# Kernel optimization log

Measured on AMD Instinct MI355X. Metric: run time of the kernel, lower is better.

## Reference

```python
import jax, jax.numpy as jnp
import numpy as np

PAD = 0  # module-level global in the original repo (MT convention)


def setup_inputs() -> dict:
    key = jax.random.key(0)
    k1, k2, k3 = jax.random.split(key, 3)
    N, V, D = 2048, 32000, 512
    # realistic log-probabilities over the vocab
    pred_ll = jax.nn.log_softmax(jax.random.normal(k1, (N, V), jnp.float32), axis=-1)
    target = jax.random.randint(k2, (N,), 0, V)
    # frozen pretrained word-vector table (nn.Embedding.from_pretrained)
    emb = jax.random.normal(k3, (V, D), jnp.float32)
    return {"pred_ll": pred_ll, "target": target, "emb": emb}


def reference(pred_ll, target, emb):
    # pred_ll: [N, V] log-probs; target: [N] int ids; emb: [V, D] frozen table
    mask = (target != PAD).astype(pred_ll.dtype)  # [N] non-pad mask

    # nll_loss = -pred_ll.gather(-1, target) summed over non-pad tokens
    nll = -jnp.take_along_axis(pred_ll, target[:, None], axis=-1)[:, 0]  # [N]
    nll_loss = jnp.sum(nll * mask)

    # pairwise L2 distance gold-embedding vs full table, via the GEMM identity
    # ||g - e||^2 = ||g||^2 + ||e||^2 - 2 g.e  (avoids the [N, V, D] tensor)
    g = emb[target]                                    # [N, D]
    g2 = jnp.sum(g * g, axis=-1, keepdims=True)        # [N, 1]
    e2 = jnp.sum(emb * emb, axis=-1)[None, :]          # [1, V]
    d2 = jnp.maximum(g2 + e2 - 2.0 * (g @ emb.T), 0.0)  # [N, V]
    dist = jnp.sqrt(jnp.maximum(d2, 1e-12))             # [N, V], L2 distances

    dist_max = jnp.max(dist, axis=1, keepdims=True)    # [N, 1]
    w = jax.nn.softmax(dist_max - jnp.abs(dist), axis=1)  # [N, V]

    # loss = sum_v softmax_weight * (-log p), summed over non-pad tokens
    loss = jnp.sum(w * (-pred_ll), axis=1)             # [N]
    return (jnp.sum(loss * mask), nll_loss)
```

## Files before the change

kernel.cpp:

```cpp
#include <hip/hip_runtime.h>
#include <float.h>

#define NTOK   2048
#define VOCAB  32000
#define DIM    512
#define NCHUNK 32
#define NTILES 2000
#define ROWSB  64
#define NRB    (NTOK / ROWSB)
#define TILE_BYTES 8192

typedef __attribute__((ext_vector_type(4))) float f32x4;
typedef unsigned int u32;
typedef long long i64;

__device__ __forceinline__ i64 pack_fp8x8(f32x4 x0, f32x4 x1) {
    int lo = __builtin_amdgcn_cvt_pk_fp8_f32(x0.x, x0.y, 0, false);
    lo = __builtin_amdgcn_cvt_pk_fp8_f32(x0.z, x0.w, lo, true);
    int hi = __builtin_amdgcn_cvt_pk_fp8_f32(x1.x, x1.y, 0, false);
    hi = __builtin_amdgcn_cvt_pk_fp8_f32(x1.z, x1.w, hi, true);
    return (i64)(((unsigned long long)(u32)hi << 32) | (u32)lo);
}

__device__ __forceinline__ void async_copy16(void* lds, const void* g) {
    __builtin_amdgcn_global_load_lds(
        (const __attribute__((address_space(1))) u32*)(const u32*)g,
        (__attribute__((address_space(3))) u32*)(u32*)lds, 16, 0, 0);
}

__global__ void init_out(float* out) {
    if (threadIdx.x < 2) out[threadIdx.x] = 0.f;
}

__global__ __launch_bounds__(256) void precast_kernel(
    const float* __restrict__ emb, char* __restrict__ Bbf, float* __restrict__ e2) {
    const int tile = blockIdx.x;
    const int t = threadIdx.x, w = t >> 6, l = t & 63;
    const int v0 = tile * 16;
    char* tbase = Bbf + (size_t)tile * TILE_BYTES;
    #pragma unroll
    for (int it = 0; it < 4; ++it) {
        const int v = it * 4 + w;
        const float* src = emb + (size_t)(v0 + v) * DIM + l * 8;
        f32x4 x0 = *(const f32x4*)src;
        f32x4 x1 = *(const f32x4*)(src + 4);
        float sq = x0.x*x0.x + x0.y*x0.y + x0.z*x0.z + x0.w*x0.w
                 + x1.x*x1.x + x1.y*x1.y + x1.z*x1.z + x1.w*x1.w;
        #pragma unroll
        for (int m = 1; m < 64; m <<= 1) sq += __shfl_xor(sq, m);
        if (l == 0) e2[v0 + v] = sq;
        *(i64*)(tbase + (l >> 2) * 512 + ((l & 3) * 16 + v) * 8) = pack_fp8x8(x0, x1);
    }
}

__global__ __launch_bounds__(256) void e2_kernel(const float* __restrict__ emb,
                                                 float* __restrict__ e2) {
    int gid = blockIdx.x * 256 + threadIdx.x;
    int wid = gid >> 6, l = gid & 63;
    if (wid >= VOCAB) return;
    const float* row = emb + (size_t)wid * DIM + l * 8;
    f32x4 a = *(const f32x4*)row;
    f32x4 b = *(const f32x4*)(row + 4);
    float s = a.x*a.x + a.y*a.y + a.z*a.z + a.w*a.w
            + b.x*b.x + b.y*b.y + b.z*b.z + b.w*b.w;
    #pragma unroll
    for (int m = 1; m < 64; m <<= 1) s += __shfl_xor(s, m);
    if (l == 0) e2[wid] = s;
}

template<bool PRECAST>
__global__ __launch_bounds__(256, 4) void fused_kernel(
    const float* __restrict__ pred_ll, const int* __restrict__ target,
    const float* __restrict__ emb, const char* __restrict__ Bbf,
    const float* __restrict__ e2g,
    float* __restrict__ partials ) {

    const int rb = blockIdx.x;
    const int ch = blockIdx.y;
    const int t  = threadIdx.x;
    const int w  = t >> 6;
    const int l  = t & 63;
    const int l15 = l & 15;
    const int lg  = l >> 4;

    __shared__ char ldsB[2][TILE_BYTES];

    const int t0 = (ch * NTILES) >> 5;
    const int t1 = ((ch + 1) * NTILES) >> 5;
    const int rowbase = rb * ROWSB + w * 16;

    i64 afrag[16];
    {
        const int grow = target[rowbase + l15];
        if constexpr (PRECAST) {
            const char* ab = Bbf + (size_t)(grow >> 4) * TILE_BYTES
                           + ((l & 48) + (grow & 15)) * 8;
            #pragma unroll
            for (int ks = 0; ks < 16; ++ks)
                afrag[ks] = *(const i64*)(ab + ks * 512);
        } else {
            const float* gsrc = emb + (size_t)grow * DIM;
            #pragma unroll
            for (int ks = 0; ks < 16; ++ks) {
                const int k0 = ks * 32 + ((l >> 4) << 3);
                afrag[ks] = pack_fp8x8(*(const f32x4*)(gsrc + k0),
                                       *(const f32x4*)(gsrc + k0 + 4));
            }
        }
    }
    float g2[4];
    #pragma unroll
    for (int r = 0; r < 4; ++r) g2[r] = e2g[target[rowbase + lg * 4 + r]];

    float s_[4] = {0.f, 0.f, 0.f, 0.f};
    float ac_[4] = {0.f, 0.f, 0.f, 0.f};

    auto stage = [&](int buf, int tg) {
        if constexpr (PRECAST) {
            const char* src = Bbf + (size_t)tg * TILE_BYTES;
            async_copy16(ldsB[buf] + t * 16, src + t * 16);
            async_copy16(ldsB[buf] + 4096 + t * 16, src + 4096 + t * 16);
        } else {
            const int v0 = tg * 16;
            #pragma unroll
            for (int it = 0; it < 4; ++it) {
                const int c = it * 256 + t;
                const int ks = c >> 6, il = c & 63;
                const int v = il & 15, k0 = ks * 32 + ((il >> 4) << 3);
                const float* src = emb + (size_t)(v0 + v) * DIM + k0;
                *(i64*)(ldsB[buf] + ks * 512 + il * 8) =
                    pack_fp8x8(*(const f32x4*)src, *(const f32x4*)(src + 4));
            }
        }
    };

    stage(0, t0);

    int cur = 0;
    #pragma unroll 1
    for (int tg = t0; tg < t1; ++tg) {
        if (tg + 1 < t1) {
            stage(cur ^ 1, tg + 1);
            if constexpr (PRECAST)
                asm volatile("s_waitcnt vmcnt(2)" ::: "memory");
            else
                asm volatile("s_waitcnt vmcnt(0) lgkmcnt(0)" ::: "memory");
        } else {
            asm volatile("s_waitcnt vmcnt(0) lgkmcnt(0)" ::: "memory");
        }
        __builtin_amdgcn_s_barrier();

        const int v0 = tg * 16;
        const float e2v = e2g[v0 + l15];
        float q[4];
        {
            const size_t p0 = (size_t)rowbase * VOCAB + v0 + l15;
            #pragma unroll
            for (int r = 0; r < 4; ++r)
                q[r] = pred_ll[p0 + (size_t)(lg * 4 + r) * VOCAB];
        }

        f32x4 acc = {0.f, 0.f, 0.f, 0.f};
        const char* lb = ldsB[cur];
        #pragma unroll
        for (int ks = 0; ks < 16; ++ks) {
            const i64 b = *(const i64*)(lb + ks * 512 + l * 8);
            acc = __builtin_amdgcn_mfma_f32_16x16x32_fp8_fp8(afrag[ks], b, acc, 0, 0, 0);
        }

        #pragma unroll
        for (int r = 0; r < 4; ++r) {
            float d2 = fmaxf(fmaf(-2.f, acc[r], g2[r] + e2v), 1e-12f);
            const float e = __expf(-sqrtf(d2));
            s_[r] += e;
            ac_[r] = fmaf(e, -q[r], ac_[r]);
        }

        asm volatile("" ::: "memory");
        __builtin_amdgcn_s_barrier();
        cur ^= 1;
    }

    #pragma unroll
    for (int r = 0; r < 4; ++r) {
        float sv = s_[r], av = ac_[r];
        #pragma unroll
        for (int m = 1; m < 16; m <<= 1) {
            sv += __shfl_xor(sv, m);
            av += __shfl_xor(av, m);
        }
        if (l15 == 0) {
            const int rg = rowbase + lg * 4 + r;
            float* pp = partials + ((size_t)rg * NCHUNK + ch) * 2;
            pp[0] = sv; pp[1] = av;
        }
    }
}

__global__ __launch_bounds__(256) void reduce_kernel(
    const float* __restrict__ pred_ll, const int* __restrict__ target,
    const float* __restrict__ partials, float* __restrict__ out) {
    const int row = blockIdx.x * 256 + threadIdx.x;
    float loss = 0.f, nll = 0.f;
    if (row < NTOK) {
        const int tg = target[row];
        const float mask = (tg != 0) ? 1.f : 0.f;
        const float* pp = partials + (size_t)row * NCHUNK * 2;
        float S = 0.f, A = 0.f;
        #pragma unroll 8
        for (int c = 0; c < NCHUNK; ++c) { S += pp[c * 2]; A += pp[c * 2 + 1]; }
        loss = mask * (A / S);
        nll  = mask * (-pred_ll[(size_t)row * VOCAB + tg]);
    }
    #pragma unroll
    for (int o = 32; o > 0; o >>= 1) {
        loss += __shfl_xor(loss, o);
        nll  += __shfl_xor(nll, o);
    }
    if ((threadIdx.x & 63) == 0) {
        atomicAdd(&out[0], loss);
        atomicAdd(&out[1], nll);
    }
}

extern "C" void kernel_launch(void* const* d_in, const int* in_sizes, int n_in,
                              void* d_out, int out_size, void* d_ws, size_t ws_size,
                              hipStream_t stream) {
    const float* pred_ll = (const float*)d_in[0];
    const int*   target  = (const int*)d_in[1];
    const float* emb     = (const float*)d_in[2];
    float* out = (float*)d_out;

    float* e2       = (float*)d_ws;
    float* partials = e2 + VOCAB;
    const size_t base = (size_t)VOCAB * 4 + (size_t)NTOK * NCHUNK * 2 * 4;
    char* Bbf       = (char*)d_ws + base;
    const size_t need = base + (size_t)NTILES * TILE_BYTES;
    const bool precast = (ws_size >= need);

    hipLaunchKernelGGL(init_out, dim3(1), dim3(64), 0, stream, out);
    if (precast) {
        hipLaunchKernelGGL(precast_kernel, dim3(NTILES), dim3(256), 0, stream, emb, Bbf, e2);
        hipLaunchKernelGGL((fused_kernel<true>), dim3(NRB, NCHUNK), dim3(256), 0, stream,
                           pred_ll, target, emb, Bbf, e2, partials);
    } else {
        hipLaunchKernelGGL(e2_kernel, dim3(VOCAB * 64 / 256), dim3(256), 0, stream, emb, e2);
        hipLaunchKernelGGL((fused_kernel<false>), dim3(NRB, NCHUNK), dim3(256), 0, stream,
                           pred_ll, target, emb, Bbf, e2, partials);
    }
    hipLaunchKernelGGL(reduce_kernel, dim3(NTOK / 256), dim3(256), 0, stream,
                       pred_ll, target, partials, out);
}
```

Before: 151.1 us.

## Enlarge fused GEMM tile to 32x32 per wave with 2x2 MFMA blocking

Each wave now handles 32 rows and a 32-column vocab tile, computing four 16x16 fp8 MFMA blocks per k-step so A fragments and LDS B reads are reused twice. The precast layout, staging (four async copies per tile), chunk count and row-block size change to match, and launch bounds drop to 3 waves per SIMD. The goal is fewer LDS reads and barriers per MFMA and less B-tile traffic per row. The cost is higher register pressure (32 A fragments, 16 accumulators) and lower occupancy, which may hurt latency hiding of the strided pred_ll loads.

Result: slower. 157.5 us (+4.2%).

```diff
diff --git a/kernel.cpp b/kernel.cpp
--- a/kernel.cpp
+++ b/kernel.cpp
@@ -4,11 +4,11 @@
 #define NTOK   2048
 #define VOCAB  32000
 #define DIM    512
-#define NCHUNK 32
-#define NTILES 2000
-#define ROWSB  64
+#define NCHUNK 64
+#define NT32   (VOCAB / 32)
+#define ROWSB  128
 #define NRB    (NTOK / ROWSB)
-#define TILE_BYTES 8192
+#define TILE_BYTES 16384
 
 typedef __attribute__((ext_vector_type(4))) float f32x4;
 typedef unsigned int u32;
@@ -36,10 +36,10 @@
     const float* __restrict__ emb, char* __restrict__ Bbf, float* __restrict__ e2) {
     const int tile = blockIdx.x;
     const int t = threadIdx.x, w = t >> 6, l = t & 63;
-    const int v0 = tile * 16;
+    const int v0 = tile * 32;
     char* tbase = Bbf + (size_t)tile * TILE_BYTES;
     #pragma unroll
-    for (int it = 0; it < 4; ++it) {
+    for (int it = 0; it < 8; ++it) {
         const int v = it * 4 + w;
         const float* src = emb + (size_t)(v0 + v) * DIM + l * 8;
         f32x4 x0 = *(const f32x4*)src;
@@ -49,7 +49,8 @@
         #pragma unroll
         for (int m = 1; m < 64; m <<= 1) sq += __shfl_xor(sq, m);
         if (l == 0) e2[v0 + v] = sq;
-        *(i64*)(tbase + (l >> 2) * 512 + ((l & 3) * 16 + v) * 8) = pack_fp8x8(x0, x1);
+        *(i64*)(tbase + (l >> 2) * 1024 + (v >> 4) * 512
+                + (((l & 3) * 16 + (v & 15)) * 8)) = pack_fp8x8(x0, x1);
     }
 }
 
@@ -69,7 +70,7 @@
 }
 
 template<bool PRECAST>
-__global__ __launch_bounds__(256, 4) void fused_kernel(
+__global__ __launch_bounds__(256, 3) void fused_kernel(
     const float* __restrict__ pred_ll, const int* __restrict__ target,
     const float* __restrict__ emb, const char* __restrict__ Bbf,
     const float* __restrict__ e2g,
@@ -85,50 +86,57 @@
 
     __shared__ char ldsB[2][TILE_BYTES];
 
-    const int t0 = (ch * NTILES) >> 5;
-    const int t1 = ((ch + 1) * NTILES) >> 5;
-    const int rowbase = rb * ROWSB + w * 16;
-
-    i64 afrag[16];
-    {
-        const int grow = target[rowbase + l15];
+    const int t0 = (ch * NT32) >> 6;
+    const int t1 = ((ch + 1) * NT32) >> 6;
+    const int rowbase = rb * ROWSB + w * 32;
+
+    i64 afrag[2][16];
+    #pragma unroll
+    for (int rs = 0; rs < 2; ++rs) {
+        const int grow = target[rowbase + rs * 16 + l15];
         if constexpr (PRECAST) {
-            const char* ab = Bbf + (size_t)(grow >> 4) * TILE_BYTES
+            const char* ab = Bbf + (size_t)(grow >> 5) * TILE_BYTES
+                           + ((grow & 31) >> 4) * 512
                            + ((l & 48) + (grow & 15)) * 8;
             #pragma unroll
             for (int ks = 0; ks < 16; ++ks)
-                afrag[ks] = *(const i64*)(ab + ks * 512);
+                afrag[rs][ks] = *(const i64*)(ab + ks * 1024);
         } else {
             const float* gsrc = emb + (size_t)grow * DIM;
             #pragma unroll
             for (int ks = 0; ks < 16; ++ks) {
                 const int k0 = ks * 32 + ((l >> 4) << 3);
-                afrag[ks] = pack_fp8x8(*(const f32x4*)(gsrc + k0),
-                                       *(const f32x4*)(gsrc + k0 + 4));
-            }
-        }
-    }
-    float g2[4];
-    #pragma unroll
-    for (int r = 0; r < 4; ++r) g2[r] = e2g[target[rowbase + lg * 4 + r]];
-
-    float s_[4] = {0.f, 0.f, 0.f, 0.f};
-    float ac_[4] = {0.f, 0.f, 0.f, 0.f};
+                afrag[rs][ks] = pack_fp8x8(*(const f32x4*)(gsrc + k0),
+                                           *(const f32x4*)(gsrc + k0 + 4));
+            }
+        }
+    }
+    float g2[2][4];
+    #pragma unroll
+    for (int rs = 0; rs < 2; ++rs)
+        #pragma unroll
+        for (int r = 0; r < 4; ++r)
+            g2[rs][r] = e2g[target[rowbase + rs * 16 + lg * 4 + r]];
+
+    float s_[2][4] = {{0,0,0,0},{0,0,0,0}};
+    float ac_[2][4] = {{0,0,0,0},{0,0,0,0}};
 
     auto stage = [&](int buf, int tg) {
         if constexpr (PRECAST) {
             const char* src = Bbf + (size_t)tg * TILE_BYTES;
-            async_copy16(ldsB[buf] + t * 16, src + t * 16);
-            async_copy16(ldsB[buf] + 4096 + t * 16, src + 4096 + t * 16);
+            #pragma unroll
+            for (int it = 0; it < 4; ++it)
+                async_copy16(ldsB[buf] + it * 4096 + t * 16, src + it * 4096 + t * 16);
         } else {
-            const int v0 = tg * 16;
-            #pragma unroll
-            for (int it = 0; it < 4; ++it) {
-                const int c = it * 256 + t;
-                const int ks = c >> 6, il = c & 63;
-                const int v = il & 15, k0 = ks * 32 + ((il >> 4) << 3);
+            const int v0 = tg * 32;
+            #pragma unroll
+            for (int it = 0; it < 8; ++it) {
+                const int slot = it * 256 + t;
+                const int ks = slot >> 7, c = (slot >> 6) & 1, il = slot & 63;
+                const int v = c * 16 + (il & 15);
+                const int k0 = ks * 32 + ((il >> 4) << 3);
                 const float* src = emb + (size_t)(v0 + v) * DIM + k0;
-                *(i64*)(ldsB[buf] + ks * 512 + il * 8) =
+                *(i64*)(ldsB[buf] + ks * 1024 + c * 512 + il * 8) =
                     pack_fp8x8(*(const f32x4*)src, *(const f32x4*)(src + 4));
             }
         }
@@ -142,7 +150,7 @@
         if (tg + 1 < t1) {
             stage(cur ^ 1, tg + 1);
             if constexpr (PRECAST)
-                asm volatile("s_waitcnt vmcnt(2)" ::: "memory");
+                asm volatile("s_waitcnt vmcnt(4)" ::: "memory");
             else
                 asm volatile("s_waitcnt vmcnt(0) lgkmcnt(0)" ::: "memory");
         } else {
@@ -150,31 +158,42 @@
         }
         __builtin_amdgcn_s_barrier();
 
-        const int v0 = tg * 16;
-        const float e2v = e2g[v0 + l15];
-        float q[4];
-        {
-            const size_t p0 = (size_t)rowbase * VOCAB + v0 + l15;
-            #pragma unroll
-            for (int r = 0; r < 4; ++r)
-                q[r] = pred_ll[p0 + (size_t)(lg * 4 + r) * VOCAB];
-        }
-
-        f32x4 acc = {0.f, 0.f, 0.f, 0.f};
+        const int v0 = tg * 32;
+        float e2v[2], q[2][2][4];
+        #pragma unroll
+        for (int cs = 0; cs < 2; ++cs) {
+            e2v[cs] = e2g[v0 + cs * 16 + l15];
+            const size_t p0 = (size_t)rowbase * VOCAB + v0 + cs * 16 + l15;
+            #pragma unroll
+            for (int rs = 0; rs < 2; ++rs)
+                #pragma unroll
+                for (int r = 0; r < 4; ++r)
+                    q[cs][rs][r] = pred_ll[p0 + (size_t)(rs * 16 + lg * 4 + r) * VOCAB];
+        }
+
+        f32x4 acc[2][2] = {{{0,0,0,0},{0,0,0,0}},{{0,0,0,0},{0,0,0,0}}};
         const char* lb = ldsB[cur];
         #pragma unroll
         for (int ks = 0; ks < 16; ++ks) {
-            const i64 b = *(const i64*)(lb + ks * 512 + l * 8);
-            acc = __builtin_amdgcn_mfma_f32_16x16x32_fp8_fp8(afrag[ks], b, acc, 0, 0, 0);
-        }
-
-        #pragma unroll
-        for (int r = 0; r < 4; ++r) {
-            float d2 = fmaxf(fmaf(-2.f, acc[r], g2[r] + e2v), 1e-12f);
-            const float e = __expf(-sqrtf(d2));
-            s_[r] += e;
-            ac_[r] = fmaf(e, -q[r], ac_[r]);
-        }
+            const i64 b0 = *(const i64*)(lb + ks * 1024 + l * 8);
+            const i64 b1 = *(const i64*)(lb + ks * 1024 + 512 + l * 8);
+            acc[0][0] = __builtin_amdgcn_mfma_f32_16x16x32_fp8_fp8(afrag[0][ks], b0, acc[0][0], 0, 0, 0);
+            acc[1][0] = __builtin_amdgcn_mfma_f32_16x16x32_fp8_fp8(afrag[1][ks], b0, acc[1][0], 0, 0, 0);
+            acc[0][1] = __builtin_amdgcn_mfma_f32_16x16x32_fp8_fp8(afrag[0][ks], b1, acc[0][1], 0, 0, 0);
+            acc[1][1] = __builtin_amdgcn_mfma_f32_16x16x32_fp8_fp8(afrag[1][ks], b1, acc[1][1], 0, 0, 0);
+        }
+
+        #pragma unroll
+        for (int cs = 0; cs < 2; ++cs)
+            #pragma unroll
+            for (int rs = 0; rs < 2; ++rs)
+                #pragma unroll
+                for (int r = 0; r < 4; ++r) {
+                    float d2 = fmaxf(fmaf(-2.f, acc[rs][cs][r], g2[rs][r] + e2v[cs]), 1e-12f);
+                    const float e = __expf(-sqrtf(d2));
+                    s_[rs][r] += e;
+                    ac_[rs][r] = fmaf(e, -q[cs][rs][r], ac_[rs][r]);
+                }
 
         asm volatile("" ::: "memory");
         __builtin_amdgcn_s_barrier();
@@ -182,19 +201,21 @@
     }
 
     #pragma unroll
-    for (int r = 0; r < 4; ++r) {
-        float sv = s_[r], av = ac_[r];
-        #pragma unroll
-        for (int m = 1; m < 16; m <<= 1) {
-            sv += __shfl_xor(sv, m);
-            av += __shfl_xor(av, m);
-        }
-        if (l15 == 0) {
-            const int rg = rowbase + lg * 4 + r;
-            float* pp = partials + ((size_t)rg * NCHUNK + ch) * 2;
-            pp[0] = sv; pp[1] = av;
-        }
-    }
+    for (int rs = 0; rs < 2; ++rs)
+        #pragma unroll
+        for (int r = 0; r < 4; ++r) {
+            float sv = s_[rs][r], av = ac_[rs][r];
+            #pragma unroll
+            for (int m = 1; m < 16; m <<= 1) {
+                sv += __shfl_xor(sv, m);
+                av += __shfl_xor(av, m);
+            }
+            if (l15 == 0) {
+                const int rg = rowbase + rs * 16 + lg * 4 + r;
+                float* pp = partials + ((size_t)rg * NCHUNK + ch) * 2;
+                pp[0] = sv; pp[1] = av;
+            }
+        }
 }
 
 __global__ __launch_bounds__(256) void reduce_kernel(
@@ -235,12 +256,12 @@
     float* partials = e2 + VOCAB;
     const size_t base = (size_t)VOCAB * 4 + (size_t)NTOK * NCHUNK * 2 * 4;
     char* Bbf       = (char*)d_ws + base;
-    const size_t need = base + (size_t)NTILES * TILE_BYTES;
+    const size_t need = base + (size_t)NT32 * TILE_BYTES;
     const bool precast = (ws_size >= need);
 
     hipLaunchKernelGGL(init_out, dim3(1), dim3(64), 0, stream, out);
     if (precast) {
-        hipLaunchKernelGGL(precast_kernel, dim3(NTILES), dim3(256), 0, stream, emb, Bbf, e2);
+        hipLaunchKernelGGL(precast_kernel, dim3(NT32), dim3(256), 0, stream, emb, Bbf, e2);
         hipLaunchKernelGGL((fused_kernel<true>), dim3(NRB, NCHUNK), dim3(256), 0, stream,
                            pred_ll, target, emb, Bbf, e2, partials);
     } else {
```

## Triple-buffer B tiles and async-stage pred_ll into LDS with more chunks

Applied to the files above, without the earlier changes.

Moves to a three-stage LDS pipeline that prefetches two tiles ahead and drops the trailing barrier. The pred_ll tile and the e2 slice are now staged asynchronously into LDS instead of being loaded straight from global memory inside the loop. The vocab split goes from 32 to 50 chunks, which gives more blocks for occupancy. The aim is to hide global-load latency for q and the B tiles behind the MFMA work. In exchange it uses more LDS per block, which may cut occupancy, and there are more partials to reduce.

Result: slower. 173.5 us (+14.8%).

```diff
diff --git a/kernel.cpp b/kernel.cpp
--- a/kernel.cpp
+++ b/kernel.cpp
@@ -4,8 +4,10 @@
 #define NTOK   2048
 #define VOCAB  32000
 #define DIM    512
-#define NCHUNK 32
-#define NTILES 2000
+#define NCHUNK 50
+#define NT16   2000
+#define TPC    (NT16 / NCHUNK)
+#define VCHUNK (VOCAB / NCHUNK)
 #define ROWSB  64
 #define NRB    (NTOK / ROWSB)
 #define TILE_BYTES 8192
@@ -83,11 +85,14 @@
     const int l15 = l & 15;
     const int lg  = l >> 4;
 
-    __shared__ char ldsB[2][TILE_BYTES];
-
-    const int t0 = (ch * NTILES) >> 5;
-    const int t1 = ((ch + 1) * NTILES) >> 5;
-    const int rowbase = rb * ROWSB + w * 16;
+    __shared__ __align__(16) char  ldsB[3][TILE_BYTES];
+    __shared__ __align__(16) char  ldsQ[3][4096];
+    __shared__ __align__(16) float e2l[VCHUNK];
+
+    const int t0 = ch * TPC, tend = t0 + TPC;
+    const int v0base = ch * VCHUNK;
+    const int rowblk = rb * ROWSB;
+    const int rowbase = rowblk + w * 16;
 
     i64 afrag[16];
     {
@@ -115,70 +120,68 @@
     float s_[4] = {0.f, 0.f, 0.f, 0.f};
     float ac_[4] = {0.f, 0.f, 0.f, 0.f};
 
-    auto stage = [&](int buf, int tg) {
+    auto stageF = [&](int buf, int tg) {
         if constexpr (PRECAST) {
-            const char* src = Bbf + (size_t)tg * TILE_BYTES;
-            async_copy16(ldsB[buf] + t * 16, src + t * 16);
-            async_copy16(ldsB[buf] + 4096 + t * 16, src + 4096 + t * 16);
+            const char* srcB = Bbf + (size_t)tg * TILE_BYTES;
+            async_copy16(ldsB[buf] + t * 16, srcB + t * 16);
+            async_copy16(ldsB[buf] + 4096 + t * 16, srcB + 4096 + t * 16);
         } else {
-            const int v0 = tg * 16;
             #pragma unroll
             for (int it = 0; it < 4; ++it) {
-                const int c = it * 256 + t;
-                const int ks = c >> 6, il = c & 63;
+                const int slot = it * 256 + t;
+                const int ks = slot >> 6, il = slot & 63;
                 const int v = il & 15, k0 = ks * 32 + ((il >> 4) << 3);
-                const float* src = emb + (size_t)(v0 + v) * DIM + k0;
+                const float* src = emb + (size_t)(tg * 16 + v) * DIM + k0;
                 *(i64*)(ldsB[buf] + ks * 512 + il * 8) =
                     pack_fp8x8(*(const f32x4*)src, *(const f32x4*)(src + 4));
             }
         }
+        const float* srcQ = pred_ll + (size_t)(rowblk + (t >> 2)) * VOCAB
+                          + tg * 16 + (t & 3) * 4;
+        async_copy16(ldsQ[buf] + t * 16, srcQ);
     };
 
-    stage(0, t0);
-
-    int cur = 0;
+    if (t < VCHUNK / 4) async_copy16(e2l + t * 4, e2g + v0base + t * 4);
+    stageF(0, t0);
+    stageF(1, t0 + 1);
+
+    int ibr = 0;
     #pragma unroll 1
-    for (int tg = t0; tg < t1; ++tg) {
-        if (tg + 1 < t1) {
-            stage(cur ^ 1, tg + 1);
+    for (int tg = t0; tg < tend; ++tg) {
+        if (tg == tend - 1) {
+            asm volatile("s_waitcnt vmcnt(0)" ::: "memory");
+        } else {
             if constexpr (PRECAST)
-                asm volatile("s_waitcnt vmcnt(2)" ::: "memory");
+                asm volatile("s_waitcnt vmcnt(3)" ::: "memory");
             else
-                asm volatile("s_waitcnt vmcnt(0) lgkmcnt(0)" ::: "memory");
-        } else {
-            asm volatile("s_waitcnt vmcnt(0) lgkmcnt(0)" ::: "memory");
+                asm volatile("s_waitcnt vmcnt(1) lgkmcnt(0)" ::: "memory");
         }
         __builtin_amdgcn_s_barrier();
-
-        const int v0 = tg * 16;
-        const float e2v = e2g[v0 + l15];
-        float q[4];
-        {
-            const size_t p0 = (size_t)rowbase * VOCAB + v0 + l15;
-            #pragma unroll
-            for (int r = 0; r < 4; ++r)
-                q[r] = pred_ll[p0 + (size_t)(lg * 4 + r) * VOCAB];
-        }
+        __builtin_amdgcn_sched_barrier(0);
+
+        const int ibw = (ibr >= 1) ? ibr - 1 : ibr + 2;
+        if (tg + 2 < tend) stageF(ibw, tg + 2);
 
         f32x4 acc = {0.f, 0.f, 0.f, 0.f};
-        const char* lb = ldsB[cur];
+        const char* lb = ldsB[ibr];
         #pragma unroll
         for (int ks = 0; ks < 16; ++ks) {
             const i64 b = *(const i64*)(lb + ks * 512 + l * 8);
             acc = __builtin_amdgcn_mfma_f32_16x16x32_fp8_fp8(afrag[ks], b, acc, 0, 0, 0);
         }
 
+        const float e2v = e2l[(tg - t0) * 16 + l15];
+        const char* lq = ldsQ[ibr];
         #pragma unroll
         for (int r = 0; r < 4; ++r) {
+            const float q = *(const float*)(lq + ((w * 16 + lg * 4 + r) * 64 + l15 * 4));
             float d2 = fmaxf(fmaf(-2.f, acc[r], g2[r] + e2v), 1e-12f);
             const float e = __expf(-sqrtf(d2));
             s_[r] += e;
-            ac_[r] = fmaf(e, -q[r], ac_[r]);
-        }
-
-        asm volatile("" ::: "memory");
-        __builtin_amdgcn_s_barrier();
-        cur ^= 1;
+            ac_[r] = fmaf(e, -q, ac_[r]);
+        }
+
+        ibr = (ibr >= 2) ? 0 : ibr + 1;
     }
 
     #pragma unroll
@@ -207,7 +210,7 @@
         const float mask = (tg != 0) ? 1.f : 0.f;
         const float* pp = partials + (size_t)row * NCHUNK * 2;
         float S = 0.f, A = 0.f;
-        #pragma unroll 8
+        #pragma unroll 5
         for (int c = 0; c < NCHUNK; ++c) { S += pp[c * 2]; A += pp[c * 2 + 1]; }
         loss = mask * (A / S);
         nll  = mask * (-pred_ll[(size_t)row * VOCAB + tg]);
@@ -235,12 +238,12 @@
     float* partials = e2 + VOCAB;
     const size_t base = (size_t)VOCAB * 4 + (size_t)NTOK * NCHUNK * 2 * 4;
     char* Bbf       = (char*)d_ws + base;
-    const size_t need = base + (size_t)NTILES * TILE_BYTES;
+    const size_t need = base + (size_t)NT16 * TILE_BYTES;
     const bool precast = (ws_size >= need);
 
     hipLaunchKernelGGL(init_out, dim3(1), dim3(64), 0, stream, out);
     if (precast) {
-        hipLaunchKernelGGL(precast_kernel, dim3(NTILES), dim3(256), 0, stream, emb, Bbf, e2);
+        hipLaunchKernelGGL(precast_kernel, dim3(NT16), dim3(256), 0, stream, emb, Bbf, e2);
         hipLaunchKernelGGL((fused_kernel<true>), dim3(NRB, NCHUNK), dim3(256), 0, stream,
                            pred_ll, target, emb, Bbf, e2, partials);
     } else {
```
